# Kernel optimization log

Measured on AMD Instinct MI355X. Metric: run time of the kernel, lower is better.

The kernel has to match this reference:

```python
import jax, jax.numpy as jnp
import numpy as np

DX = 1000.0
DY = 1000.0
EPS = 1e-8


def _weno5(qm2, qm1, q0, qp1, qp2):
    """Classic WENO5 left-biased reconstruction at the face i+1/2."""
    # candidate stencil reconstructions
    f1 = (1.0 / 3.0) * qm2 - (7.0 / 6.0) * qm1 + (11.0 / 6.0) * q0
    f2 = -(1.0 / 6.0) * qm1 + (5.0 / 6.0) * q0 + (1.0 / 3.0) * qp1
    f3 = (1.0 / 3.0) * q0 + (5.0 / 6.0) * qp1 - (1.0 / 6.0) * qp2
    # smoothness indicators
    k1, k2 = 13.0 / 12.0, 0.25
    b1 = k1 * (qm2 - 2.0 * qm1 + q0) ** 2 + k2 * (qm2 - 4.0 * qm1 + 3.0 * q0) ** 2
    b2 = k1 * (qm1 - 2.0 * q0 + qp1) ** 2 + k2 * (qm1 - qp1) ** 2
    b3 = k1 * (q0 - 2.0 * qp1 + qp2) ** 2 + k2 * (3.0 * q0 - 4.0 * qp1 + qp2) ** 2
    # nonlinear weights (ideal weights 1/10, 6/10, 3/10)
    w1 = 0.1 / (b1 + EPS) ** 2
    w2 = 0.6 / (b2 + EPS) ** 2
    w3 = 0.3 / (b3 + EPS) ** 2
    return (w1 * f1 + w2 * f2 + w3 * f3) / (w1 + w2 + w3)


def _flux_along(q, vel, axis):
    """Upwind WENO5 flux vel * q_face at faces i+1/2, one face per cell.

    fe[..., i] = flux at face between cells i and i+1 along `axis`.
    Boundary stencils use edge-replicated ghost cells.
    """
    n = q.shape[axis]
    pad = [(0, 0), (0, 0)]
    pad[axis] = (2, 3)  # left recon needs i-2..i+2, right recon needs i-1..i+3
    qp = jnp.pad(q, pad, mode='edge')

    def s(k):  # q at cell i+k, shape == q.shape
        return jax.lax.slice_in_dim(qp, 2 + k, 2 + k + n, axis=axis)

    q_left = _weno5(s(-2), s(-1), s(0), s(1), s(2))   # upwind for vel >= 0
    q_right = _weno5(s(3), s(2), s(1), s(0), s(-1))   # upwind for vel <  0 (mirrored)
    return vel * jnp.where(vel >= 0.0, q_left, q_right)


def setup_inputs() -> dict:
    key = jax.random.key(0)
    k1, k2, k3 = jax.random.split(key, 3)
    Ny, Nx = 2048, 4096
    h = jax.random.normal(k1, (Ny, Nx), dtype=jnp.float32)
    u = jax.random.normal(k2, (Ny, Nx), dtype=jnp.float32)
    v = jax.random.normal(k3, (Ny, Nx), dtype=jnp.float32)
    return {"h": h, "u": u, "v": v}


def reference(h, u, v):
    # WENO5 upwind fluxes at east (U-point) and north (V-point) faces
    fe = _flux_along(h, u, axis=1)
    fn = _flux_along(h, v, axis=0)
    # tendency -div(h u_vec) on the ghost=2 interior, zero on the ghost ring
    div = (fe[2:-2, 2:-2] - fe[2:-2, 1:-3]) / DX + (fn[2:-2, 2:-2] - fn[1:-3, 2:-2]) / DY
    out = jnp.zeros_like(h).at[2:-2, 2:-2].set(-div)
    return out
```

## Files before the change

kernel.cpp:

```cpp
#include <hip/hip_runtime.h>

#define NX 4096
#define NY 2048
#define EPS 1e-8f
#define CPW 63
#define INV_D 0.001f

typedef float f32x2 __attribute__((ext_vector_type(2)));

__device__ __forceinline__ int clampi(int i, int lo, int hi) {
    return i < lo ? lo : (i > hi ? hi : i);
}

__device__ __forceinline__ float weno5_s(float qm2, float qm1, float q0,
                                         float qp1, float qp2) {
    float f1 = fmaf(1.0f/3.0f, qm2, fmaf(-7.0f/6.0f, qm1, (11.0f/6.0f)*q0));
    float f2 = fmaf(-1.0f/6.0f, qm1, fmaf(5.0f/6.0f, q0, (1.0f/3.0f)*qp1));
    float f3 = fmaf(1.0f/3.0f, q0, fmaf(5.0f/6.0f, qp1, (-1.0f/6.0f)*qp2));
    const float k1 = 13.0f/12.0f, k2 = 0.25f;
    float d1 = qm2 - 2.0f*qm1 + q0,  e1 = qm2 - 4.0f*qm1 + 3.0f*q0;
    float d2 = qm1 - 2.0f*q0 + qp1,  e2 = qm1 - qp1;
    float d3 = q0 - 2.0f*qp1 + qp2,  e3 = 3.0f*q0 - 4.0f*qp1 + qp2;
    float b1 = fmaf(k1, d1*d1, k2*(e1*e1));
    float b2 = fmaf(k1, d2*d2, k2*(e2*e2));
    float b3 = fmaf(k1, d3*d3, k2*(e3*e3));
    float t1 = b1 + EPS, t2 = b2 + EPS, t3 = b3 + EPS;
    float p23 = t2*t3, p13 = t1*t3, p12 = t1*t2;
    float w1 = 0.1f*(p23*p23), w2 = 0.6f*(p13*p13), w3 = 0.3f*(p12*p12);
    float num = fmaf(w1, f1, fmaf(w2, f2, w3*f3));
    return num * __builtin_amdgcn_rcpf((w1 + w2) + w3);
}

__device__ __forceinline__ f32x2 weno5_pk(f32x2 qm2, f32x2 qm1, f32x2 q0,
                                          f32x2 qp1, f32x2 qp2) {
    f32x2 f1 = (1.0f/3.0f)*qm2 - (7.0f/6.0f)*qm1 + (11.0f/6.0f)*q0;
    f32x2 f2 = (-1.0f/6.0f)*qm1 + (5.0f/6.0f)*q0 + (1.0f/3.0f)*qp1;
    f32x2 f3 = (1.0f/3.0f)*q0 + (5.0f/6.0f)*qp1 - (1.0f/6.0f)*qp2;
    f32x2 d1 = qm2 - 2.0f*qm1 + q0;
    f32x2 e1 = qm2 - 4.0f*qm1 + 3.0f*q0;
    f32x2 d2 = qm1 - 2.0f*q0 + qp1;
    f32x2 e2 = qm1 - qp1;
    f32x2 d3 = q0 - 2.0f*qp1 + qp2;
    f32x2 e3 = 3.0f*q0 - 4.0f*qp1 + qp2;
    const float k1 = 13.0f/12.0f, k2 = 0.25f;
    f32x2 b1 = k1*(d1*d1) + k2*(e1*e1);
    f32x2 b2 = k1*(d2*d2) + k2*(e2*e2);
    f32x2 b3 = k1*(d3*d3) + k2*(e3*e3);
    f32x2 t1 = b1 + EPS, t2 = b2 + EPS, t3 = b3 + EPS;
    f32x2 p23 = t2*t3, p13 = t1*t3, p12 = t1*t2;
    f32x2 w1 = 0.1f*(p23*p23);
    f32x2 w2 = 0.6f*(p13*p13);
    f32x2 w3 = 0.3f*(p12*p12);
    f32x2 num = w1*f1 + w2*f2 + w3*f3;
    f32x2 den = (w1 + w2) + w3;
    f32x2 rc;
    rc.x = __builtin_amdgcn_rcpf(den.x);
    rc.y = __builtin_amdgcn_rcpf(den.y);
    return num * rc;
}

template <bool EDGE>
__device__ __forceinline__ void run_strip(const float* __restrict__ h,
                                          const float* __restrict__ u,
                                          const float* __restrict__ v,
                                          float* __restrict__ out,
                                          int x0, int y0w, int lane) {
    const int xf = x0 - 1 + lane;
    const int xo = x0 + lane;
    const int xc = EDGE ? (xo < NX ? xo : NX - 1) : xo;
    const int xq = EDGE ? clampi(xf, 0, NX - 1) : xf;

    int xs[6];
    if (EDGE) {
#pragma unroll
        for (int k = 0; k < 6; ++k) xs[k] = clampi(xf - 2 + k, 0, NX - 1);
    }

    float C0, C1, C2, C5, C6, C7;
    if (EDGE) {
        C0 = h[(size_t)clampi(y0w - 3, 0, NY - 1) * NX + xc];
        C1 = h[(size_t)clampi(y0w - 2, 0, NY - 1) * NX + xc];
        C2 = h[(size_t)clampi(y0w - 1, 0, NY - 1) * NX + xc];
        C5 = h[(size_t)clampi(y0w + 2, 0, NY - 1) * NX + xc];
        C6 = h[(size_t)clampi(y0w + 3, 0, NY - 1) * NX + xc];
        C7 = h[(size_t)clampi(y0w + 4, 0, NY - 1) * NX + xc];
    } else {
        const float* hc = h + (size_t)y0w * NX + xc;
        C0 = hc[-3 * NX]; C1 = hc[-2 * NX]; C2 = hc[-NX];
        C5 = hc[2 * NX];  C6 = hc[3 * NX];  C7 = hc[4 * NX];
    }
    float st0[6], st1[6];
    {
        const float* hr0 = h + (size_t)y0w * NX;
        const float* hr1 = hr0 + NX;
        if (EDGE) {
#pragma unroll
            for (int k = 0; k < 6; ++k) { st0[k] = hr0[xs[k]]; st1[k] = hr1[xs[k]]; }
        } else {
#pragma unroll
            for (int k = 0; k < 6; ++k) { st0[k] = hr0[xf - 2 + k]; st1[k] = hr1[xf - 2 + k]; }
        }
    }
    float u0 = u[(size_t)y0w * NX + xq];
    float u1 = u[(size_t)(y0w + 1) * NX + xq];
    float va, vb, vcv;
    {
        int fy = EDGE ? clampi(y0w - 1, 0, NY - 1) : (y0w - 1);
        va  = v[(size_t)fy * NX + xc];
        vb  = v[(size_t)y0w * NX + xc];
        vcv = v[(size_t)(y0w + 1) * NX + xc];
    }

    const float C3 = st0[3];
    const float C4 = st1[3];

    bool p0 = (va >= 0.0f), p1 = (vb >= 0.0f), p2 = (vcv >= 0.0f);
    f32x2 a = { p0 ? C0 : C5, p1 ? C1 : C6 };
    f32x2 b = { p0 ? C1 : C4, p1 ? C2 : C5 };
    f32x2 c = { p0 ? C2 : C3, p1 ? C3 : C4 };
    f32x2 d = { p0 ? C3 : C2, p1 ? C4 : C3 };
    f32x2 e = { p0 ? C4 : C1, p1 ? C5 : C2 };
    f32x2 qn = weno5_pk(a, b, c, d, e);
    float f0 = va * qn.x;
    float f1 = vb * qn.y;
    float f2 = vcv * weno5_s(p2 ? C2 : C7, p2 ? C3 : C6, p2 ? C4 : C5,
                             p2 ? C5 : C4, p2 ? C6 : C3);

    bool t0 = (u0 >= 0.0f), t1 = (u1 >= 0.0f);
    a = { t0 ? st0[0] : st0[5], t1 ? st1[0] : st1[5] };
    b = { t0 ? st0[1] : st0[4], t1 ? st1[1] : st1[4] };
    c = { t0 ? st0[2] : st0[3], t1 ? st1[2] : st1[3] };
    d = { t0 ? st0[3] : st0[2], t1 ? st1[3] : st1[2] };
    e = { t0 ? st0[4] : st0[1], t1 ? st1[4] : st1[1] };
    f32x2 qe = weno5_pk(a, b, c, d, e);
    float fe0 = u0 * qe.x;
    float fe1 = u1 * qe.y;
    float fe0r = __shfl_down(fe0, 1);
    float fe1r = __shfl_down(fe1, 1);

    float val0 = ((fe0 - fe0r) + (f0 - f1)) * INV_D;
    float val1 = ((fe1 - fe1r) + (f1 - f2)) * INV_D;

    if (EDGE) {
        if (xo < 2 || xo >= NX - 2 || y0w < 2 || y0w >= NY - 2) val0 = 0.0f;
        if (xo < 2 || xo >= NX - 2 || y0w + 1 < 2 || y0w + 1 >= NY - 2) val1 = 0.0f;
        if (lane < CPW && xo < NX) {
            __builtin_nontemporal_store(val0, out + (size_t)y0w * NX + xo);
            __builtin_nontemporal_store(val1, out + (size_t)(y0w + 1) * NX + xo);
        }
    } else {
        if (lane < CPW) {
            __builtin_nontemporal_store(val0, out + (size_t)y0w * NX + xo);
            __builtin_nontemporal_store(val1, out + (size_t)(y0w + 1) * NX + xo);
        }
    }
}

__global__ __launch_bounds__(256) void adv_kernel(const float* __restrict__ h,
                                                  const float* __restrict__ u,
                                                  const float* __restrict__ v,
                                                  float* __restrict__ out) {
    const int lane = threadIdx.x & 63;
    const int wid  = threadIdx.x >> 6;
    const int x0 = blockIdx.x * CPW;
    const int y0w = blockIdx.y * 8 + wid * 2;

    const bool edge = (blockIdx.x == 0) || (blockIdx.x >= 64) ||
                      (blockIdx.y == 0) || (blockIdx.y == gridDim.y - 1);
    if (edge)
        run_strip<true>(h, u, v, out, x0, y0w, lane);
    else
        run_strip<false>(h, u, v, out, x0, y0w, lane);
}

extern "C" void kernel_launch(void* const* d_in, const int* in_sizes, int n_in,
                              void* d_out, int out_size, void* d_ws, size_t ws_size,
                              hipStream_t stream) {
    const float* h = (const float*)d_in[0];
    const float* u = (const float*)d_in[1];
    const float* v = (const float*)d_in[2];
    float* out = (float*)d_out;

    dim3 block(256, 1, 1);
    dim3 grid((NX + CPW - 1) / CPW, NY / 8, 1);
    adv_kernel<<<grid, block, 0, stream>>>(h, u, v, out);
}
```

Measured before the change: 40.77 us.

## Share north-face fluxes between waves via LDS instead of recomputing

Each wave previously computed three north-face WENO5 fluxes for its two rows, one of them duplicating the face already computed by the wave below. Now each wave computes only its own two faces and publishes the upper one in shared memory. Only wave 0 computes the extra bottom face and loads the extra h row and v value it needs. The change cuts redundant WENO arithmetic and some loads, but adds a block-wide barrier and LDS traffic, and wave 0 now does extra work, which creates imbalance.

```diff
diff --git a/kernel.cpp b/kernel.cpp
--- a/kernel.cpp
+++ b/kernel.cpp
@@ -64,7 +64,9 @@
                                           const float* __restrict__ u,
                                           const float* __restrict__ v,
                                           float* __restrict__ out,
-                                          int x0, int y0w, int lane) {
+                                          float (*fsh)[64],
+                                          int x0, int yA, int lane, int wid) {
+    const int yB = yA + 1;
     const int xf = x0 - 1 + lane;
     const int xo = x0 + lane;
     const int xc = EDGE ? (xo < NX ? xo : NX - 1) : xo;
@@ -76,22 +78,31 @@
         for (int k = 0; k < 6; ++k) xs[k] = clampi(xf - 2 + k, 0, NX - 1);
     }
 
-    float C0, C1, C2, C5, C6, C7;
+    float Cm2, Cm1, Cp2, Cp3, Cp4;
     if (EDGE) {
-        C0 = h[(size_t)clampi(y0w - 3, 0, NY - 1) * NX + xc];
-        C1 = h[(size_t)clampi(y0w - 2, 0, NY - 1) * NX + xc];
-        C2 = h[(size_t)clampi(y0w - 1, 0, NY - 1) * NX + xc];
-        C5 = h[(size_t)clampi(y0w + 2, 0, NY - 1) * NX + xc];
-        C6 = h[(size_t)clampi(y0w + 3, 0, NY - 1) * NX + xc];
-        C7 = h[(size_t)clampi(y0w + 4, 0, NY - 1) * NX + xc];
+        Cm2 = h[(size_t)clampi(yA - 2, 0, NY - 1) * NX + xc];
+        Cm1 = h[(size_t)clampi(yA - 1, 0, NY - 1) * NX + xc];
+        Cp2 = h[(size_t)clampi(yA + 2, 0, NY - 1) * NX + xc];
+        Cp3 = h[(size_t)clampi(yA + 3, 0, NY - 1) * NX + xc];
+        Cp4 = h[(size_t)clampi(yA + 4, 0, NY - 1) * NX + xc];
     } else {
-        const float* hc = h + (size_t)y0w * NX + xc;
-        C0 = hc[-3 * NX]; C1 = hc[-2 * NX]; C2 = hc[-NX];
-        C5 = hc[2 * NX];  C6 = hc[3 * NX];  C7 = hc[4 * NX];
+        const float* hc = h + (size_t)yA * NX + xc;
+        Cm2 = hc[-2 * NX]; Cm1 = hc[-NX];
+        Cp2 = hc[2 * NX];  Cp3 = hc[3 * NX]; Cp4 = hc[4 * NX];
+    }
+    float Cm3 = 0.0f, vm = 0.0f;
+    if (wid == 0) {
+        if (EDGE) {
+            Cm3 = h[(size_t)clampi(yA - 3, 0, NY - 1) * NX + xc];
+            vm  = v[(size_t)clampi(yA - 1, 0, NY - 1) * NX + xc];
+        } else {
+            Cm3 = h[(size_t)(yA - 3) * NX + xc];
+            vm  = v[(size_t)(yA - 1) * NX + xc];
+        }
     }
     float st0[6], st1[6];
     {
-        const float* hr0 = h + (size_t)y0w * NX;
+        const float* hr0 = h + (size_t)yA * NX;
         const float* hr1 = hr0 + NX;
         if (EDGE) {
 #pragma unroll
@@ -101,30 +112,31 @@
             for (int k = 0; k < 6; ++k) { st0[k] = hr0[xf - 2 + k]; st1[k] = hr1[xf - 2 + k]; }
         }
     }
-    float u0 = u[(size_t)y0w * NX + xq];
-    float u1 = u[(size_t)(y0w + 1) * NX + xq];
-    float va, vb, vcv;
-    {
-        int fy = EDGE ? clampi(y0w - 1, 0, NY - 1) : (y0w - 1);
-        va  = v[(size_t)fy * NX + xc];
-        vb  = v[(size_t)y0w * NX + xc];
-        vcv = v[(size_t)(y0w + 1) * NX + xc];
-    }
-
-    const float C3 = st0[3];
-    const float C4 = st1[3];
-
-    bool p0 = (va >= 0.0f), p1 = (vb >= 0.0f), p2 = (vcv >= 0.0f);
-    f32x2 a = { p0 ? C0 : C5, p1 ? C1 : C6 };
-    f32x2 b = { p0 ? C1 : C4, p1 ? C2 : C5 };
-    f32x2 c = { p0 ? C2 : C3, p1 ? C3 : C4 };
-    f32x2 d = { p0 ? C3 : C2, p1 ? C4 : C3 };
-    f32x2 e = { p0 ? C4 : C1, p1 ? C5 : C2 };
+    float u0 = u[(size_t)yA * NX + xq];
+    float u1 = u[(size_t)yB * NX + xq];
+    float vA = v[(size_t)yA * NX + xc];
+    float vB = v[(size_t)yB * NX + xc];
+
+    const float CA = st0[3];
+    const float CB = st1[3];
+
+    bool pA = (vA >= 0.0f), pB = (vB >= 0.0f);
+    f32x2 a = { pA ? Cm2 : Cp3, pB ? Cm1 : Cp4 };
+    f32x2 b = { pA ? Cm1 : Cp2, pB ? CA  : Cp3 };
+    f32x2 c = { pA ? CA  : CB,  pB ? CB  : Cp2 };
+    f32x2 d = { pA ? CB  : CA,  pB ? Cp2 : CB  };
+    f32x2 e = { pA ? Cp2 : Cm1, pB ? Cp3 : CA  };
     f32x2 qn = weno5_pk(a, b, c, d, e);
-    float f0 = va * qn.x;
-    float f1 = vb * qn.y;
-    float f2 = vcv * weno5_s(p2 ? C2 : C7, p2 ? C3 : C6, p2 ? C4 : C5,
-                             p2 ? C5 : C4, p2 ? C6 : C3);
+    float fnA = vA * qn.x;
+    float fnB = vB * qn.y;
+
+    float fn_m1 = 0.0f;
+    if (wid == 0) {
+        bool pm = (vm >= 0.0f);
+        fn_m1 = vm * weno5_s(pm ? Cm3 : Cp2, pm ? Cm2 : CB, pm ? Cm1 : CA,
+                             pm ? CA : Cm1,  pm ? CB : Cm2);
+    }
+    if (wid < 3) fsh[wid][lane] = fnB;
 
     bool t0 = (u0 >= 0.0f), t1 = (u1 >= 0.0f);
     a = { t0 ? st0[0] : st0[5], t1 ? st1[0] : st1[5] };
@@ -138,20 +150,23 @@
     float fe0r = __shfl_down(fe0, 1);
     float fe1r = __shfl_down(fe1, 1);
 
-    float val0 = ((fe0 - fe0r) + (f0 - f1)) * INV_D;
-    float val1 = ((fe1 - fe1r) + (f1 - f2)) * INV_D;
+    __syncthreads();
+    float fn_below = (wid == 0) ? fn_m1 : fsh[wid - 1][lane];
+
+    float val0 = ((fe0 - fe0r) + (fn_below - fnA)) * INV_D;
+    float val1 = ((fe1 - fe1r) + (fnA - fnB)) * INV_D;
 
     if (EDGE) {
-        if (xo < 2 || xo >= NX - 2 || y0w < 2 || y0w >= NY - 2) val0 = 0.0f;
-        if (xo < 2 || xo >= NX - 2 || y0w + 1 < 2 || y0w + 1 >= NY - 2) val1 = 0.0f;
+        if (xo < 2 || xo >= NX - 2 || yA < 2 || yA >= NY - 2) val0 = 0.0f;
+        if (xo < 2 || xo >= NX - 2 || yB < 2 || yB >= NY - 2) val1 = 0.0f;
         if (lane < CPW && xo < NX) {
-            __builtin_nontemporal_store(val0, out + (size_t)y0w * NX + xo);
-            __builtin_nontemporal_store(val1, out + (size_t)(y0w + 1) * NX + xo);
+            __builtin_nontemporal_store(val0, out + (size_t)yA * NX + xo);
+            __builtin_nontemporal_store(val1, out + (size_t)yB * NX + xo);
         }
     } else {
         if (lane < CPW) {
-            __builtin_nontemporal_store(val0, out + (size_t)y0w * NX + xo);
-            __builtin_nontemporal_store(val1, out + (size_t)(y0w + 1) * NX + xo);
+            __builtin_nontemporal_store(val0, out + (size_t)yA * NX + xo);
+            __builtin_nontemporal_store(val1, out + (size_t)yB * NX + xo);
         }
     }
 }
@@ -160,17 +175,18 @@
                                                   const float* __restrict__ u,
                                                   const float* __restrict__ v,
                                                   float* __restrict__ out) {
+    __shared__ float fsh[3][64];
     const int lane = threadIdx.x & 63;
     const int wid  = threadIdx.x >> 6;
     const int x0 = blockIdx.x * CPW;
-    const int y0w = blockIdx.y * 8 + wid * 2;
+    const int yA = blockIdx.y * 8 + wid * 2;
 
     const bool edge = (blockIdx.x == 0) || (blockIdx.x >= 64) ||
                       (blockIdx.y == 0) || (blockIdx.y == gridDim.y - 1);
     if (edge)
-        run_strip<true>(h, u, v, out, x0, y0w, lane);
+        run_strip<true>(h, u, v, out, fsh, x0, yA, lane, wid);
     else
-        run_strip<false>(h, u, v, out, x0, y0w, lane);
+        run_strip<false>(h, u, v, out, fsh, x0, yA, lane, wid);
 }
 
 extern "C" void kernel_launch(void* const* d_in, const int* in_sizes, int n_in,
```

After: 39.99 us. About the same (-1.9%).
